# Performance work log

Measured on AMD Instinct MI355X. Metric: run time of the kernel, lower is better.

The kernel has to match this reference:

```python
import jax, jax.numpy as jnp
import numpy as np

B, C, H, W = 8, 512, 32, 32
N = H * W            # grid cells
G = 256              # num_groups
R = 9                # relations (self + 8 neighbors)
EPS = 1e-7           # module's self.eps
BN_EPS = 1e-5        # torch BatchNorm default eps


def setup_inputs() -> dict:
    key = jax.random.key(0)
    ks = jax.random.split(key, 10)
    inp = jax.random.normal(ks[0], (B, C, H, W), jnp.float32)
    group_label = jax.random.randint(ks[1], (B, N), 0, G)
    adj_mats = jax.random.uniform(ks[2], (R, N, N), jnp.float32)
    w1 = jax.random.normal(ks[3], (3, C, C), jnp.float32) * 0.02
    wg = jax.random.normal(ks[4], (3, R * C, R * C), jnp.float32) * 0.02
    w2 = jax.random.normal(ks[5], (3, C, C), jnp.float32) * 0.02
    bn_gamma = jnp.ones((3, 3, G), jnp.float32)
    bn_beta = jnp.zeros((3, 3, G), jnp.float32)
    conv_w = jax.random.normal(ks[6], (C, 2 * C), jnp.float32) * 0.02
    conv_b = jnp.zeros((C,), jnp.float32)
    return {"inp": inp, "group_label": group_label, "adj_mats": adj_mats,
            "w1": w1, "wg": wg, "w2": w2, "bn_gamma": bn_gamma,
            "bn_beta": bn_beta, "conv_w": conv_w, "conv_b": conv_b}


def _batchnorm(x, gamma, beta):
    # x: (B, G, C); BatchNorm1d(num_features=G): normalize over (B, C) per group
    mean = jnp.mean(x, axis=(0, 2), keepdims=True)
    var = jnp.var(x, axis=(0, 2), keepdims=True)
    return gamma[None, :, None] * (x - mean) * jax.lax.rsqrt(var + BN_EPS) + beta[None, :, None]


def _res_block(x, coef, w1, wg, w2, gam, bet):
    # x: (B, G, C); coef: (B, 9, G, G)
    h = x @ w1.T                                  # dense1 (no bias)
    h = jax.nn.relu(_batchnorm(h, gam[0], bet[0]))
    e = jnp.tile(h, (1, 1, R)) @ wg.T             # (B, G, 9C) graph_conv_1
    e = e.reshape(B, R, G, C)                     # same row-major reinterpret as torch
    h = jnp.einsum('brgh,brhc->bgc', coef, e)     # coef @ out, then sum over relations
    h = jax.nn.relu(_batchnorm(h, gam[1], bet[1]))
    h = h @ w2.T                                  # dense2 (no bias)
    h = _batchnorm(h, gam[2], bet[2]) + x
    return jax.nn.relu(h)


def reference(inp, group_label, adj_mats, w1, wg, w2, bn_gamma, bn_beta, conv_w, conv_b):
    gm = jax.nn.one_hot(group_label, G, dtype=inp.dtype)        # (B, N, G)
    # make_coef_matrix
    t = jnp.einsum('rnm,bmg->brng', adj_mats, gm)               # (B, 9, N, G)
    ga = jnp.einsum('brng,bnh->brgh', t, gm)                    # (B, 9, G, G)
    den = jax.nn.relu(ga - jnp.flip(ga, axis=0))                # flip over batch dim (as in source)
    den = den.at[:, 3].set(ga[:, 3])
    coef = den / (ga.sum(axis=3, keepdims=True) + 1.0)          # (B, 9, G, G)
    # pooling
    bar = gm / (gm.sum(axis=2, keepdims=True) + EPS)
    x = jnp.einsum('bcn,bng->bgc', inp.reshape(B, C, N), bar)   # (B, G, C)
    # three residual blocks
    for i in range(3):
        x = _res_block(x, coef, w1[i], wg[i], w2[i], bn_gamma[i], bn_beta[i])
    # unpooling
    tilde = gm / (gm.sum(axis=1, keepdims=True) + EPS)
    x = jnp.einsum('bng,bgc->bnc', tilde, x).reshape(B, C, H, W)  # raw reshape as in torch
    xcat = jnp.concatenate([x, inp], axis=1)                      # (B, 2C, H, W)
    out = jnp.einsum('bchw,oc->bohw', xcat, conv_w) + conv_b[None, :, None, None]
    return out
```

## Files before the change

### kernel.cpp

```cpp
#include <hip/hip_runtime.h>
#include <math.h>

using half8 = __attribute__((ext_vector_type(8))) _Float16;
using half4 = __attribute__((ext_vector_type(4))) _Float16;
using f32x4 = __attribute__((ext_vector_type(4))) float;

static constexpr size_t OFF_WGCH  = 0;
static constexpr size_t OFF_COEF  = 7077888;
static constexpr size_t OFF_COEFH = 11796480;
static constexpr size_t OFF_X     = 16515072;
static constexpr size_t OFF_CNTI  = 17565696;
static constexpr size_t OFF_LISTS = 17567744;
static constexpr size_t OFF_CSRO  = 17666048;
static constexpr size_t OFF_CSRV  = 17668352;
static constexpr size_t OFF_W1H   = 17672960;
static constexpr size_t OFF_W2H   = 18459392;
static constexpr size_t OFF_CWH   = 19245824;
static constexpr size_t OFF_XH    = 19770112;
static constexpr size_t OFF_HH    = 20818688;
static constexpr size_t OFF_BIG   = 21867264;
static constexpr size_t OFF_GA    = 40741632;
static constexpr size_t OFF_H1    = OFF_GA;
static constexpr size_t OFF_H2    = OFF_GA + 1048576;

__device__ inline void gll16(const void* g, void* l) {
  __builtin_amdgcn_global_load_lds(
      (__attribute__((address_space(1))) void*)(size_t)g,
      (__attribute__((address_space(3))) void*)(size_t)l, 16, 0, 0);
}

__global__ __launch_bounds__(256) void k_collapse_wg(const float* __restrict__ wg,
                                                     _Float16* __restrict__ whi) {
  size_t idx = (size_t)blockIdx.x * 256 + threadIdx.x;
  size_t i = idx / (4608u * 128u);
  size_t rem = idx % (4608u * 128u);
  size_t j = rem / 128u, c4 = rem % 128u;
  const float* p = wg + i * 21233664ull + j * 4608ull + c4 * 4;
  float4 s = {0.f, 0.f, 0.f, 0.f};
#pragma unroll
  for (int r = 0; r < 9; ++r) {
    float4 v = *(const float4*)(p + r * 512);
    s.x += v.x; s.y += v.y; s.z += v.z; s.w += v.w;
  }
  half4 hv;
  hv[0] = (_Float16)s.x; hv[1] = (_Float16)s.y;
  hv[2] = (_Float16)s.z; hv[3] = (_Float16)s.w;
  *(half4*)&whi[idx * 4] = hv;
}

__global__ __launch_bounds__(256) void k_split3(const float* __restrict__ w1,
                                                const float* __restrict__ w2,
                                                const float* __restrict__ cw,
                                                _Float16* __restrict__ w1h,
                                                _Float16* __restrict__ w2h,
                                                _Float16* __restrict__ cwh) {
  size_t idx = (size_t)blockIdx.x * 256 + threadIdx.x;
  if (idx < 786432) {
    w1h[idx] = (_Float16)w1[idx];
  } else if (idx < 1572864) {
    size_t o = idx - 786432;
    w2h[o] = (_Float16)w2[o];
  } else {
    size_t o = idx - 1572864;
    cwh[o] = (_Float16)cw[o];
  }
}

__global__ __launch_bounds__(256) void k_lists(const int* __restrict__ gl,
                                               int* __restrict__ cntI,
                                               int* __restrict__ lists) {
  int idx = blockIdx.x * 256 + threadIdx.x;
  int b = idx >> 10, n = idx & 1023;
  int h = gl[idx];
  int pos = atomicAdd(&cntI[b * 256 + h], 1);
  if (pos < 48) lists[(b * 256 + h) * 48 + pos] = n;
}

__global__ __launch_bounds__(256) void k_csr(const int* __restrict__ cntI,
                                             const int* __restrict__ lists,
                                             int* __restrict__ csr_off,
                                             unsigned short* __restrict__ csr_val) {
  __shared__ int wsum[256];
  __shared__ int tot[257];
  int t = threadIdx.x;
  int base = t * 8;
  int loc[8]; int s = 0;
#pragma unroll
  for (int i = 0; i < 8; ++i) {
    int c = cntI[base + i]; if (c > 48) c = 48;
    loc[i] = s; s += c;
  }
  wsum[t] = s;
  __syncthreads();
  if (t == 0) {
    int a = 0;
    for (int i = 0; i < 256; ++i) { tot[i] = a; a += wsum[i]; }
    tot[256] = a;
  }
  __syncthreads();
  int off0 = tot[t];
#pragma unroll
  for (int i = 0; i < 8; ++i) {
    int bg = base + i;
    int o = off0 + loc[i];
    csr_off[bg] = o;
    int c = cntI[bg]; if (c > 48) c = 48;
    for (int j = 0; j < c; ++j)
      csr_val[o + j] = (unsigned short)(lists[bg * 48 + j] & 1023);
  }
  if (t == 0) csr_off[2048] = tot[256];
}

__global__ __launch_bounds__(256) void k_t2ga(const float* __restrict__ adj,
                                              const int* __restrict__ cntI,
                                              const int* __restrict__ lists,
                                              float* __restrict__ gaT) {
  __shared__ float ul[9][1024];
  __shared__ int lsh[48];
  int t = threadIdx.x;
  int b = blockIdx.x >> 8, h = blockIdx.x & 255;
  int cnt = cntI[b * 256 + h]; if (cnt > 48) cnt = 48;
  if (t < cnt) lsh[t] = lists[(b * 256 + h) * 48 + t];
  __syncthreads();
  float u[9][4];
#pragma unroll
  for (int r = 0; r < 9; ++r)
#pragma unroll
    for (int j = 0; j < 4; ++j) u[r][j] = 0.f;
  for (int i = 0; i < cnt; ++i) {
    const float* base = adj + ((size_t)lsh[i] << 10) + t;
#pragma unroll
    for (int r = 0; r < 9; ++r) {
      const float* p = base + (size_t)r * 1048576;
      u[r][0] += p[0];
      u[r][1] += p[256];
      u[r][2] += p[512];
      u[r][3] += p[768];
    }
  }
#pragma unroll
  for (int r = 0; r < 9; ++r)
#pragma unroll
    for (int j = 0; j < 4; ++j) ul[r][j * 256 + t] = u[r][j];
  __syncthreads();
  int g = t;
  int cg = cntI[b * 256 + g]; if (cg > 48) cg = 48;
  const int* lg = lists + (b * 256 + g) * 48;
  float s[9];
#pragma unroll
  for (int r = 0; r < 9; ++r) s[r] = 0.f;
  for (int i = 0; i < cg; ++i) {
    int m = lg[i];
#pragma unroll
    for (int r = 0; r < 9; ++r) s[r] += ul[r][m];
  }
#pragma unroll
  for (int r = 0; r < 9; ++r)
    gaT[(((size_t)(b * 9 + r)) * 256 + h) * 256 + g] = s[r];
}

__global__ __launch_bounds__(256) void k_gasum(const float* __restrict__ gaT,
                                               float* __restrict__ rowsum) {
  int z = blockIdx.x;
  int t = threadIdx.x;
  const float* p = gaT + ((size_t)z * 256) * 256 + t;
  float s = 0.f;
  for (int h = 0; h < 256; ++h) s += p[(size_t)h * 256];
  rowsum[z * 256 + t] = s;
}

__global__ __launch_bounds__(256) void k_coef_t(const float* __restrict__ gaT,
                                                const float* __restrict__ rowsum,
                                                _Float16* __restrict__ chi) {
  __shared__ float tl[64][65];
  __shared__ float tlf[64][65];
  __shared__ float rs[64];
  int t = threadIdx.x;
  int z = blockIdx.y;
  int b = z / 9, r = z % 9;
  int tile = blockIdx.x;
  int h0 = (tile & 3) * 64, g0 = (tile >> 2) * 64;
  size_t base  = ((size_t)z * 256 + h0) * 256 + g0;
  size_t baseF = ((size_t)((7 - b) * 9 + r) * 256 + h0) * 256 + g0;
  for (int k = t; k < 4096; k += 256) {
    int i = k >> 6, j = k & 63;
    tl[i][j]  = gaT[base  + (size_t)i * 256 + j];
    tlf[i][j] = gaT[baseF + (size_t)i * 256 + j];
  }
  if (t < 64) rs[t] = rowsum[z * 256 + g0 + t] + 1.0f;
  __syncthreads();
  for (int k = t; k < 4096; k += 256) {
    int i2 = k >> 6, j2 = k & 63;
    float v = tl[j2][i2], vf = tlf[j2][i2];
    float num = (r == 3) ? v : fmaxf(v - vf, 0.f);
    float c = num / rs[i2];
    size_t o = ((size_t)z * 256 + g0 + i2) * 256 + h0 + j2;
    chi[o] = (_Float16)c;
  }
}

__global__ __launch_bounds__(256) void k_pool_csr(const float* __restrict__ inp,
                                                  const int* __restrict__ csr_off,
                                                  const unsigned short* __restrict__ csr_val,
                                                  float* __restrict__ x,
                                                  _Float16* __restrict__ xh) {
  __shared__ float rows[8][1032];
  __shared__ int offs[257];
  __shared__ unsigned short vals[1024];
  int t = threadIdx.x;
  int b = blockIdx.x >> 6, cch = blockIdx.x & 63;
  const float4* src = (const float4*)(inp + (size_t)b * 524288 + (size_t)cch * 8 * 1024);
  for (int k = t; k < 2048; k += 256) {
    float4 v = src[k];
    int c = k >> 8;
    int m = (k & 255) << 2;
    *(float4*)&rows[c][m] = v;
  }
  for (int k = t; k < 257; k += 256) offs[k] = csr_off[b * 256 + k];
  __syncthreads();
  int vbase = offs[0];
  int nv = offs[256] - vbase;
  for (int k = t; k < nv; k += 256) vals[k] = csr_val[vbase + k];
  __syncthreads();
  int g = t;
  int o0 = offs[g] - vbase, o1 = offs[g + 1] - vbase;
  float s[8] = {0.f, 0.f, 0.f, 0.f, 0.f, 0.f, 0.f, 0.f};
  for (int i = o0; i < o1; ++i) {
    int n = vals[i];
#pragma unroll
    for (int c = 0; c < 8; ++c) s[c] += rows[c][n];
  }
  const float sc = 1.0f / (1.0f + 1e-7f);
  size_t xbase = ((size_t)b * 256 + g) * 512 + cch * 8;
#pragma unroll
  for (int c = 0; c < 8; ++c) {
    float v = s[c] * sc;
    x[xbase + c] = v;
    xh[xbase + c] = (_Float16)v;
  }
}

__global__ __launch_bounds__(256) void k_mfma_nt1f(const _Float16* __restrict__ Ahi,
                                                   const _Float16* __restrict__ Bhi,
                                                   float* __restrict__ C,
                                                   const float* __restrict__ bias,
                                                   int M, int N, int K,
                                                   size_t Bbs, size_t Cbs) {
  __shared__ __align__(16) _Float16 Ash[2][128][32];
  __shared__ __align__(16) _Float16 Bsh[2][64][32];
  int tid = threadIdx.x;
  int z = blockIdx.z;
  const _Float16* Bh = Bhi + (size_t)z * Bbs;
  float* Cz = C + (size_t)z * Cbs;
  int bm = blockIdx.y * 128, bn = blockIdx.x * 64;
  int w = tid >> 6, lane = tid & 63;
  int wr = w >> 1, wc = w & 1;
  int l15 = lane & 15, l4 = lane >> 4;
  int rsub = lane >> 2;
  int qk = (lane & 3) * 8;
  int ar = w * 16 + rsub;
  int ar2 = ar + 64;
  f32x4 acc[4][2];
#pragma unroll
  for (int m = 0; m < 4; ++m)
#pragma unroll
    for (int n = 0; n < 2; ++n) acc[m][n] = (f32x4){0.f, 0.f, 0.f, 0.f};
  auto STG = [&](int bi, int k0) {
    gll16(Ahi + (size_t)(bm + ar) * K + k0 + qk,  &Ash[bi][w * 16][0]);
    gll16(Ahi + (size_t)(bm + ar2) * K + k0 + qk, &Ash[bi][w * 16 + 64][0]);
    gll16(Bh + (size_t)(bn + ar) * K + k0 + qk,   &Bsh[bi][w * 16][0]);
  };
  int nt = K >> 5;
  STG(0, 0);
  int cur = 0;
  for (int t = 0; t < nt; ++t, cur ^= 1) {
    __syncthreads();
    if (t + 1 < nt) STG(cur ^ 1, (t + 1) << 5);
    half8 afh[4], bfh[2];
#pragma unroll
    for (int m = 0; m < 4; ++m)
      afh[m] = *(const half8*)&Ash[cur][wr * 64 + m * 16 + l15][l4 * 8];
#pragma unroll
    for (int n = 0; n < 2; ++n)
      bfh[n] = *(const half8*)&Bsh[cur][wc * 32 + n * 16 + l15][l4 * 8];
#pragma unroll
    for (int m = 0; m < 4; ++m)
#pragma unroll
      for (int n = 0; n < 2; ++n)
        acc[m][n] = __builtin_amdgcn_mfma_f32_16x16x32_f16(afh[m], bfh[n], acc[m][n], 0, 0, 0);
  }
#pragma unroll
  for (int m = 0; m < 4; ++m)
#pragma unroll
    for (int n = 0; n < 2; ++n)
#pragma unroll
      for (int rr = 0; rr < 4; ++rr) {
        int row = bm + wr * 64 + m * 16 + l4 * 4 + rr;
        int col = bn + wc * 32 + n * 16 + l15;
        float v = acc[m][n][rr];
        if (bias) v += bias[row];
        Cz[(size_t)row * N + col] = v;
      }
}

__global__ __launch_bounds__(256) void k_mfma_nt1f_64(const _Float16* __restrict__ Ahi,
                                                      const _Float16* __restrict__ Bhi,
                                                      _Float16* __restrict__ C,
                                                      int M, int N, int K) {
  __shared__ __align__(16) _Float16 Ash[2][64][32];
  __shared__ __align__(16) _Float16 Bsh[2][64][32];
  int tid = threadIdx.x;
  int bm = blockIdx.y * 64, bn = blockIdx.x * 64;
  int w = tid >> 6, lane = tid & 63;
  int wr = w >> 1, wc = w & 1;
  int l15 = lane & 15, l4 = lane >> 4;
  int rsub = lane >> 2;
  int qk = (lane & 3) * 8;
  int ar = w * 16 + rsub;
  f32x4 acc[2][2];
#pragma unroll
  for (int m = 0; m < 2; ++m)
#pragma unroll
    for (int n = 0; n < 2; ++n) acc[m][n] = (f32x4){0.f, 0.f, 0.f, 0.f};
  auto STG = [&](int bi, int k0) {
    gll16(Ahi + (size_t)(bm + ar) * K + k0 + qk, &Ash[bi][w * 16][0]);
    gll16(Bhi + (size_t)(bn + ar) * K + k0 + qk, &Bsh[bi][w * 16][0]);
  };
  int nt = K >> 5;
  STG(0, 0);
  int cur = 0;
  for (int t = 0; t < nt; ++t, cur ^= 1) {
    __syncthreads();
    if (t + 1 < nt) STG(cur ^ 1, (t + 1) << 5);
    half8 afh[2], bfh[2];
#pragma unroll
    for (int m = 0; m < 2; ++m)
      afh[m] = *(const half8*)&Ash[cur][wr * 32 + m * 16 + l15][l4 * 8];
#pragma unroll
    for (int n = 0; n < 2; ++n)
      bfh[n] = *(const half8*)&Bsh[cur][wc * 32 + n * 16 + l15][l4 * 8];
#pragma unroll
    for (int m = 0; m < 2; ++m)
#pragma unroll
      for (int n = 0; n < 2; ++n)
        acc[m][n] = __builtin_amdgcn_mfma_f32_16x16x32_f16(afh[m], bfh[n], acc[m][n], 0, 0, 0);
  }
#pragma unroll
  for (int m = 0; m < 2; ++m)
#pragma unroll
    for (int n = 0; n < 2; ++n)
#pragma unroll
      for (int rr = 0; rr < 4; ++rr) {
        int row = bm + wr * 32 + m * 16 + l4 * 4 + rr;
        int col = bn + wc * 32 + n * 16 + l15;
        C[(size_t)row * N + col] = (_Float16)acc[m][n][rr];
      }
}

__global__ __launch_bounds__(256) void k_mfma_nt1f_128(const _Float16* __restrict__ Ahi,
                                                       const _Float16* __restrict__ Bhi,
                                                       _Float16* __restrict__ C,
                                                       int M, int N, int K) {
  __shared__ __align__(16) _Float16 Ash[2][128][32];
  __shared__ __align__(16) _Float16 Bsh[2][128][32];
  int tid = threadIdx.x;
  int bm = blockIdx.y * 128, bn = blockIdx.x * 128;
  int w = tid >> 6, lane = tid & 63;
  int wr = w >> 1, wc = w & 1;
  int l15 = lane & 15, l4 = lane >> 4;
  int rsub = lane >> 2;
  int qk = (lane & 3) * 8;
  int ar = w * 16 + rsub;
  int ar2 = ar + 64;
  f32x4 acc[4][4];
#pragma unroll
  for (int m = 0; m < 4; ++m)
#pragma unroll
    for (int n = 0; n < 4; ++n) acc[m][n] = (f32x4){0.f, 0.f, 0.f, 0.f};
  auto STG = [&](int bi, int k0) {
    gll16(Ahi + (size_t)(bm + ar) * K + k0 + qk,  &Ash[bi][w * 16][0]);
    gll16(Ahi + (size_t)(bm + ar2) * K + k0 + qk, &Ash[bi][w * 16 + 64][0]);
    gll16(Bhi + (size_t)(bn + ar) * K + k0 + qk,  &Bsh[bi][w * 16][0]);
    gll16(Bhi + (size_t)(bn + ar2) * K + k0 + qk, &Bsh[bi][w * 16 + 64][0]);
  };
  int nt = K >> 5;
  STG(0, 0);
  int cur = 0;
  for (int t = 0; t < nt; ++t, cur ^= 1) {
    __syncthreads();
    if (t + 1 < nt) STG(cur ^ 1, (t + 1) << 5);
    half8 afh[4], bfh[4];
#pragma unroll
    for (int m = 0; m < 4; ++m)
      afh[m] = *(const half8*)&Ash[cur][wr * 64 + m * 16 + l15][l4 * 8];
#pragma unroll
    for (int n = 0; n < 4; ++n)
      bfh[n] = *(const half8*)&Bsh[cur][wc * 64 + n * 16 + l15][l4 * 8];
#pragma unroll
    for (int m = 0; m < 4; ++m)
#pragma unroll
      for (int n = 0; n < 4; ++n)
        acc[m][n] = __builtin_amdgcn_mfma_f32_16x16x32_f16(afh[m], bfh[n], acc[m][n], 0, 0, 0);
  }
#pragma unroll
  for (int m = 0; m < 4; ++m)
#pragma unroll
    for (int n = 0; n < 4; ++n)
#pragma unroll
      for (int rr = 0; rr < 4; ++rr) {
        int row = bm + wr * 64 + m * 16 + l4 * 4 + rr;
        int col = bn + wc * 64 + n * 16 + l15;
        C[(size_t)row * N + col] = (_Float16)acc[m][n][rr];
      }
}

__global__ __launch_bounds__(256) void k_eT_split(const _Float16* __restrict__ e,
                                                  _Float16* __restrict__ eth) {
  __shared__ _Float16 tl[64][72];
  int t = threadIdx.x;
  int z = blockIdx.z;
  int b = z / 9, r = z % 9;
  int h0 = blockIdx.y * 64, c0 = blockIdx.x * 64;
  const _Float16* ez = e + (size_t)b * 1179648 + (size_t)r * 131072;
  for (int k = t; k < 4096; k += 256) {
    int i = k >> 6, j = k & 63;
    tl[i][j] = ez[(size_t)(h0 + i) * 512 + c0 + j];
  }
  __syncthreads();
  for (int k = t; k < 4096; k += 256) {
    int i = k >> 6, j = k & 63;
    size_t o = ((size_t)z * 512 + c0 + i) * 256 + h0 + j;
    eth[o] = tl[j][i];
  }
}

__global__ __launch_bounds__(256) void k_einsum_mfma(const _Float16* __restrict__ Ahi,
                                                     const _Float16* __restrict__ Bhi,
                                                     _Float16* __restrict__ h2) {
  __shared__ __align__(16) _Float16 Ash[2][64][32];
  __shared__ __align__(16) _Float16 Bsh[2][64][32];
  int tid = threadIdx.x;
  int b = blockIdx.z;
  int bm = blockIdx.y * 64, bn = blockIdx.x * 64;
  int w = tid >> 6, lane = tid & 63;
  int wr = w >> 1, wc = w & 1;
  int l15 = lane & 15, l4 = lane >> 4;
  int rsub = lane >> 2;
  int qk = (lane & 3) * 8;
  int ar = w * 16 + rsub;
  f32x4 acc[2][2];
#pragma unroll
  for (int m = 0; m < 2; ++m)
#pragma unroll
    for (int n = 0; n < 2; ++n) acc[m][n] = (f32x4){0.f, 0.f, 0.f, 0.f};
  auto STG = [&](int bi, int kk) {
    int r = kk >> 3, k0 = (kk & 7) << 5;
    const _Float16* Ah = Ahi + ((size_t)b * 9 + r) * 65536 + (size_t)(bm + ar) * 256 + k0 + qk;
    const _Float16* Bh = Bhi + ((size_t)b * 9 + r) * 131072 + (size_t)(bn + ar) * 256 + k0 + qk;
    gll16(Ah, &Ash[bi][w * 16][0]);
    gll16(Bh, &Bsh[bi][w * 16][0]);
  };
  STG(0, 0);
  int cur = 0;
  for (int kk = 0; kk < 72; ++kk, cur ^= 1) {
    __syncthreads();
    if (kk + 1 < 72) STG(cur ^ 1, kk + 1);
    half8 afh[2], bfh[2];
#pragma unroll
    for (int m = 0; m < 2; ++m)
      afh[m] = *(const half8*)&Ash[cur][wr * 32 + m * 16 + l15][l4 * 8];
#pragma unroll
    for (int n = 0; n < 2; ++n)
      bfh[n] = *(const half8*)&Bsh[cur][wc * 32 + n * 16 + l15][l4 * 8];
#pragma unroll
    for (int m = 0; m < 2; ++m)
#pragma unroll
      for (int n = 0; n < 2; ++n)
        acc[m][n] = __builtin_amdgcn_mfma_f32_16x16x32_f16(afh[m], bfh[n], acc[m][n], 0, 0, 0);
  }
#pragma unroll
  for (int m = 0; m < 2; ++m)
#pragma unroll
    for (int n = 0; n < 2; ++n)
#pragma unroll
      for (int rr = 0; rr < 4; ++rr) {
        int row = bm + wr * 32 + m * 16 + l4 * 4 + rr;
        int col = bn + wc * 32 + n * 16 + l15;
        h2[(size_t)b * 131072 + (size_t)row * 512 + col] = (_Float16)acc[m][n][rr];
      }
}

__global__ __launch_bounds__(256) void k_bn_fused(const _Float16* __restrict__ h,
                                                  const float* __restrict__ gamma,
                                                  const float* __restrict__ beta,
                                                  float* __restrict__ x,
                                                  _Float16* __restrict__ ohi,
                                                  int res) {
  __shared__ double ls[256], lq[256];
  __shared__ float bc[2];
  int g = blockIdx.x;
  int tid = threadIdx.x;
  float v[16];
  double s = 0.0, q = 0.0;
#pragma unroll
  for (int i = 0; i < 16; ++i) {
    int idx = i * 256 + tid;
    int bb = idx >> 9, c = idx & 511;
    float f = (float)h[((size_t)(bb * 256 + g) << 9) + c];
    v[i] = f;
    double d = (double)f;
    s += d; q += d * d;
  }
  ls[tid] = s; lq[tid] = q;
  __syncthreads();
  for (int off = 128; off; off >>= 1) {
    if (tid < off) { ls[tid] += ls[tid + off]; lq[tid] += lq[tid + off]; }
    __syncthreads();
  }
  if (tid == 0) {
    double mean = ls[0] * (1.0 / 4096.0);
    double var = lq[0] * (1.0 / 4096.0) - mean * mean;
    if (var < 0.0) var = 0.0;
    float rstd = (float)rsqrt(var + 1e-5);
    float a = gamma[g] * rstd;
    bc[0] = a;
    bc[1] = beta[g] - (float)mean * a;
  }
  __syncthreads();
  float a = bc[0], b2 = bc[1];
#pragma unroll
  for (int i = 0; i < 16; ++i) {
    int idx = i * 256 + tid;
    int bb = idx >> 9, c = idx & 511;
    size_t o = ((size_t)(bb * 256 + g) << 9) + c;
    float y = fmaf(v[i], a, b2);
    if (res) y += x[o];
    y = fmaxf(y, 0.f);
    if (res) x[o] = y;
    ohi[o] = (_Float16)y;
  }
}

__global__ __launch_bounds__(256) void k_xcatT(const float* __restrict__ x,
                                               const int* __restrict__ cntI,
                                               const int* __restrict__ gl,
                                               const float* __restrict__ inp,
                                               _Float16* __restrict__ xch) {
  __shared__ float tl[64][65];
  __shared__ int lab[1024];
  __shared__ float ic[256];
  int t = threadIdx.x;
  int b = blockIdx.y, p0 = blockIdx.x * 64;
  if (blockIdx.z == 0) {
    for (int k = t; k < 1024; k += 256) lab[k] = gl[b * 1024 + k];
    if (t < 256) ic[t] = 1.0f / ((float)cntI[b * 256 + t] + 1e-7f);
    __syncthreads();
    for (int pp = 0; pp < 64; ++pp) {
      int p = p0 + pp;
      int p9 = p >> 9, c2 = p & 511;
      const float* xb = x + (size_t)b * 131072 + c2;
      size_t obase = ((size_t)b * 1024 + p) * 1024;
#pragma unroll
      for (int ch = 0; ch < 512; ch += 256) {
        int c = ch + t;
        int g = lab[2 * c + p9];
        xch[obase + c] = (_Float16)(xb[(size_t)g * 512] * ic[g]);
      }
    }
  } else {
    for (int ct = 0; ct < 512; ct += 64) {
      __syncthreads();
      for (int k = t; k < 4096; k += 256) {
        int i = k >> 6, j = k & 63;
        tl[i][j] = inp[(size_t)b * 524288 + (size_t)(ct + i) * 1024 + p0 + j];
      }
      __syncthreads();
      for (int k = t; k < 4096; k += 256) {
        int i = k >> 6, j = k & 63;
        size_t o = ((size_t)b * 1024 + p0 + i) * 1024 + 512 + ct + j;
        xch[o] = (_Float16)tl[j][i];
      }
    }
  }
}

extern "C" void kernel_launch(void* const* d_in, const int* in_sizes, int n_in,
                              void* d_out, int out_size, void* d_ws, size_t ws_size,
                              hipStream_t stream) {
  const float* inp   = (const float*)d_in[0];
  const int*   gl    = (const int*)d_in[1];
  const float* adj   = (const float*)d_in[2];
  const float* w1    = (const float*)d_in[3];
  const float* wg    = (const float*)d_in[4];
  const float* w2    = (const float*)d_in[5];
  const float* bng   = (const float*)d_in[6];
  const float* bnb   = (const float*)d_in[7];
  const float* convw = (const float*)d_in[8];
  const float* convb = (const float*)d_in[9];
  float* out = (float*)d_out;
  float* ws = (float*)d_ws;

  _Float16* wgchi = (_Float16*)(ws + OFF_WGCH);
  _Float16* coefhi = (_Float16*)(ws + OFF_COEFH);
  float* rowsum = ws + OFF_COEF;
  float* x     = ws + OFF_X;
  int*   cntI  = (int*)(ws + OFF_CNTI);
  int*   lists = (int*)(ws + OFF_LISTS);
  int*   csrO  = (int*)(ws + OFF_CSRO);
  unsigned short* csrV = (unsigned short*)(ws + OFF_CSRV);
  _Float16* w1hi = (_Float16*)(ws + OFF_W1H);
  _Float16* w2hi = (_Float16*)(ws + OFF_W2H);
  _Float16* cwhi = (_Float16*)(ws + OFF_CWH);
  _Float16* xhi  = (_Float16*)(ws + OFF_XH);
  _Float16* hhi  = (_Float16*)(ws + OFF_HH);
  _Float16* e_h  = (_Float16*)(ws + OFF_BIG);
  _Float16* eth  = (_Float16*)(ws + OFF_BIG + 4718592);
  _Float16* xch  = (_Float16*)(ws + OFF_BIG);
  float* gaT = ws + OFF_GA;
  _Float16* h1h = (_Float16*)(ws + OFF_H1);
  _Float16* h2h = (_Float16*)(ws + OFF_H2);

  hipMemsetAsync(cntI, 0, 2048 * 4, stream);

  k_collapse_wg<<<6912, 256, 0, stream>>>(wg, wgchi);
  k_split3<<<8192, 256, 0, stream>>>(w1, w2, convw, w1hi, w2hi, cwhi);
  k_lists<<<32, 256, 0, stream>>>(gl, cntI, lists);
  k_csr<<<1, 256, 0, stream>>>(cntI, lists, csrO, csrV);
  k_t2ga<<<2048, 256, 0, stream>>>(adj, cntI, lists, gaT);
  k_gasum<<<72, 256, 0, stream>>>(gaT, rowsum);
  k_coef_t<<<dim3(16, 72), 256, 0, stream>>>(gaT, rowsum, coefhi);
  k_pool_csr<<<512, 256, 0, stream>>>(inp, csrO, csrV, x, xhi);

  for (int i = 0; i < 3; ++i) {
    k_mfma_nt1f_64<<<dim3(8, 32), 256, 0, stream>>>(xhi, w1hi + (size_t)i * 262144,
        h1h, 2048, 512, 512);
    k_bn_fused<<<256, 256, 0, stream>>>(h1h, bng + (i * 3 + 0) * 256, bnb + (i * 3 + 0) * 256,
        nullptr, hhi, 0);
    k_mfma_nt1f_128<<<dim3(36, 16), 256, 0, stream>>>(hhi, wgchi + (size_t)i * 2359296,
        e_h, 2048, 4608, 512);
    k_eT_split<<<dim3(8, 4, 72), 256, 0, stream>>>(e_h, eth);
    k_einsum_mfma<<<dim3(8, 4, 8), 256, 0, stream>>>(coefhi, eth, h2h);
    k_bn_fused<<<256, 256, 0, stream>>>(h2h, bng + (i * 3 + 1) * 256, bnb + (i * 3 + 1) * 256,
        nullptr, hhi, 0);
    k_mfma_nt1f_64<<<dim3(8, 32), 256, 0, stream>>>(hhi, w2hi + (size_t)i * 262144,
        h1h, 2048, 512, 512);
    k_bn_fused<<<256, 256, 0, stream>>>(h1h, bng + (i * 3 + 2) * 256, bnb + (i * 3 + 2) * 256,
        x, xhi, 1);
  }

  k_xcatT<<<dim3(16, 8, 2), 256, 0, stream>>>(x, cntI, gl, inp, xch);
  k_mfma_nt1f<<<dim3(16, 4, 8), 256, 0, stream>>>(cwhi, xch, out, convb,
      512, 1024, 1024, 1048576, 524288);
}
```

Before: 478.8 us.

## Double K-step per stage in MFMA GEMMs and merge weight prep kernels

All four MFMA GEMM kernels now stage 64 K-elements per pipeline step, as two 32-wide sub-tiles, instead of 32. This halves the number of __syncthreads barriers and loop iterations and gives each wave more MFMA work per barrier. The cost is double the LDS footprint, which can lower occupancy. Separately, the wg-collapse and weight-cast kernels are merged into one launch to save a kernel launch.

```diff
diff --git a/kernel.cpp b/kernel.cpp
--- a/kernel.cpp
+++ b/kernel.cpp
@@ -29,40 +29,42 @@
       (__attribute__((address_space(3))) void*)(size_t)l, 16, 0, 0);
 }
 
-__global__ __launch_bounds__(256) void k_collapse_wg(const float* __restrict__ wg,
-                                                     _Float16* __restrict__ whi) {
-  size_t idx = (size_t)blockIdx.x * 256 + threadIdx.x;
-  size_t i = idx / (4608u * 128u);
-  size_t rem = idx % (4608u * 128u);
-  size_t j = rem / 128u, c4 = rem % 128u;
-  const float* p = wg + i * 21233664ull + j * 4608ull + c4 * 4;
-  float4 s = {0.f, 0.f, 0.f, 0.f};
-#pragma unroll
-  for (int r = 0; r < 9; ++r) {
-    float4 v = *(const float4*)(p + r * 512);
-    s.x += v.x; s.y += v.y; s.z += v.z; s.w += v.w;
-  }
-  half4 hv;
-  hv[0] = (_Float16)s.x; hv[1] = (_Float16)s.y;
-  hv[2] = (_Float16)s.z; hv[3] = (_Float16)s.w;
-  *(half4*)&whi[idx * 4] = hv;
-}
-
-__global__ __launch_bounds__(256) void k_split3(const float* __restrict__ w1,
+__global__ __launch_bounds__(256) void k_prep_w(const float* __restrict__ wg,
+                                                const float* __restrict__ w1,
                                                 const float* __restrict__ w2,
                                                 const float* __restrict__ cw,
+                                                _Float16* __restrict__ wgh,
                                                 _Float16* __restrict__ w1h,
                                                 _Float16* __restrict__ w2h,
                                                 _Float16* __restrict__ cwh) {
-  size_t idx = (size_t)blockIdx.x * 256 + threadIdx.x;
-  if (idx < 786432) {
-    w1h[idx] = (_Float16)w1[idx];
-  } else if (idx < 1572864) {
-    size_t o = idx - 786432;
-    w2h[o] = (_Float16)w2[o];
+  int bid = blockIdx.x;
+  if (bid < 6912) {
+    size_t idx = (size_t)bid * 256 + threadIdx.x;
+    size_t i = idx / (4608u * 128u);
+    size_t rem = idx % (4608u * 128u);
+    size_t j = rem / 128u, c4 = rem % 128u;
+    const float* p = wg + i * 21233664ull + j * 4608ull + c4 * 4;
+    float4 s = {0.f, 0.f, 0.f, 0.f};
+#pragma unroll
+    for (int r = 0; r < 9; ++r) {
+      float4 v = *(const float4*)(p + r * 512);
+      s.x += v.x; s.y += v.y; s.z += v.z; s.w += v.w;
+    }
+    half4 hv;
+    hv[0] = (_Float16)s.x; hv[1] = (_Float16)s.y;
+    hv[2] = (_Float16)s.z; hv[3] = (_Float16)s.w;
+    *(half4*)&wgh[idx * 4] = hv;
   } else {
-    size_t o = idx - 1572864;
-    cwh[o] = (_Float16)cw[o];
+    size_t idx = (size_t)(bid - 6912) * 256 + threadIdx.x;
+    if (idx < 786432) {
+      w1h[idx] = (_Float16)w1[idx];
+    } else if (idx < 1572864) {
+      size_t o = idx - 786432;
+      w2h[o] = (_Float16)w2[o];
+    } else {
+      size_t o = idx - 1572864;
+      cwh[o] = (_Float16)cw[o];
+    }
   }
 }
 
@@ -246,8 +248,8 @@
                                                    const float* __restrict__ bias,
                                                    int M, int N, int K,
                                                    size_t Bbs, size_t Cbs) {
-  __shared__ __align__(16) _Float16 Ash[2][128][32];
-  __shared__ __align__(16) _Float16 Bsh[2][64][32];
+  __shared__ __align__(16) _Float16 Ash[2][2][128][32];
+  __shared__ __align__(16) _Float16 Bsh[2][2][64][32];
   int tid = threadIdx.x;
   int z = blockIdx.z;
   const _Float16* Bh = Bhi + (size_t)z * Bbs;
@@ -266,28 +268,35 @@
 #pragma unroll
     for (int n = 0; n < 2; ++n) acc[m][n] = (f32x4){0.f, 0.f, 0.f, 0.f};
   auto STG = [&](int bi, int k0) {
-    gll16(Ahi + (size_t)(bm + ar) * K + k0 + qk,  &Ash[bi][w * 16][0]);
-    gll16(Ahi + (size_t)(bm + ar2) * K + k0 + qk, &Ash[bi][w * 16 + 64][0]);
-    gll16(Bh + (size_t)(bn + ar) * K + k0 + qk,   &Bsh[bi][w * 16][0]);
+#pragma unroll
+    for (int ks = 0; ks < 2; ++ks) {
+      int kk = k0 + ks * 32;
+      gll16(Ahi + (size_t)(bm + ar) * K + kk + qk,  &Ash[bi][ks][w * 16][0]);
+      gll16(Ahi + (size_t)(bm + ar2) * K + kk + qk, &Ash[bi][ks][w * 16 + 64][0]);
+      gll16(Bh + (size_t)(bn + ar) * K + kk + qk,   &Bsh[bi][ks][w * 16][0]);
+    }
   };
-  int nt = K >> 5;
+  int nt = K >> 6;
   STG(0, 0);
   int cur = 0;
   for (int t = 0; t < nt; ++t, cur ^= 1) {
     __syncthreads();
-    if (t + 1 < nt) STG(cur ^ 1, (t + 1) << 5);
-    half8 afh[4], bfh[2];
-#pragma unroll
-    for (int m = 0; m < 4; ++m)
-      afh[m] = *(const half8*)&Ash[cur][wr * 64 + m * 16 + l15][l4 * 8];
-#pragma unroll
-    for (int n = 0; n < 2; ++n)
-      bfh[n] = *(const half8*)&Bsh[cur][wc * 32 + n * 16 + l15][l4 * 8];
-#pragma unroll
-    for (int m = 0; m < 4; ++m)
+    if (t + 1 < nt) STG(cur ^ 1, (t + 1) << 6);
+#pragma unroll
+    for (int ks = 0; ks < 2; ++ks) {
+      half8 afh[4], bfh[2];
+#pragma unroll
+      for (int m = 0; m < 4; ++m)
+        afh[m] = *(const half8*)&Ash[cur][ks][wr * 64 + m * 16 + l15][l4 * 8];
 #pragma unroll
       for (int n = 0; n < 2; ++n)
-        acc[m][n] = __builtin_amdgcn_mfma_f32_16x16x32_f16(afh[m], bfh[n], acc[m][n], 0, 0, 0);
+        bfh[n] = *(const half8*)&Bsh[cur][ks][wc * 32 + n * 16 + l15][l4 * 8];
+#pragma unroll
+      for (int m = 0; m < 4; ++m)
+#pragma unroll
+        for (int n = 0; n < 2; ++n)
+          acc[m][n] = __builtin_amdgcn_mfma_f32_16x16x32_f16(afh[m], bfh[n], acc[m][n], 0, 0, 0);
+    }
   }
 #pragma unroll
   for (int m = 0; m < 4; ++m)
@@ -307,8 +316,8 @@
                                                       const _Float16* __restrict__ Bhi,
                                                       _Float16* __restrict__ C,
                                                       int M, int N, int K) {
-  __shared__ __align__(16) _Float16 Ash[2][64][32];
-  __shared__ __align__(16) _Float16 Bsh[2][64][32];
+  __shared__ __align__(16) _Float16 Ash[2][2][64][32];
+  __shared__ __align__(16) _Float16 Bsh[2][2][64][32];
   int tid = threadIdx.x;
   int bm = blockIdx.y * 64, bn = blockIdx.x * 64;
   int w = tid >> 6, lane = tid & 63;
@@ -323,27 +332,34 @@
 #pragma unroll
     for (int n = 0; n < 2; ++n) acc[m][n] = (f32x4){0.f, 0.f, 0.f, 0.f};
   auto STG = [&](int bi, int k0) {
-    gll16(Ahi + (size_t)(bm + ar) * K + k0 + qk, &Ash[bi][w * 16][0]);
-    gll16(Bhi + (size_t)(bn + ar) * K + k0 + qk, &Bsh[bi][w * 16][0]);
+#pragma unroll
+    for (int ks = 0; ks < 2; ++ks) {
+      int kk = k0 + ks * 32;
+      gll16(Ahi + (size_t)(bm + ar) * K + kk + qk, &Ash[bi][ks][w * 16][0]);
+      gll16(Bhi + (size_t)(bn + ar) * K + kk + qk, &Bsh[bi][ks][w * 16][0]);
+    }
   };
-  int nt = K >> 5;
+  int nt = K >> 6;
   STG(0, 0);
   int cur = 0;
   for (int t = 0; t < nt; ++t, cur ^= 1) {
     __syncthreads();
-    if (t + 1 < nt) STG(cur ^ 1, (t + 1) << 5);
-    half8 afh[2], bfh[2];
-#pragma unroll
-    for (int m = 0; m < 2; ++m)
-      afh[m] = *(const half8*)&Ash[cur][wr * 32 + m * 16 + l15][l4 * 8];
-#pragma unroll
-    for (int n = 0; n < 2; ++n)
-      bfh[n] = *(const half8*)&Bsh[cur][wc * 32 + n * 16 + l15][l4 * 8];
-#pragma unroll
-    for (int m = 0; m < 2; ++m)
+    if (t + 1 < nt) STG(cur ^ 1, (t + 1) << 6);
+#pragma unroll
+    for (int ks = 0; ks < 2; ++ks) {
+      half8 afh[2], bfh[2];
+#pragma unroll
+      for (int m = 0; m < 2; ++m)
+        afh[m] = *(const half8*)&Ash[cur][ks][wr * 32 + m * 16 + l15][l4 * 8];
 #pragma unroll
       for (int n = 0; n < 2; ++n)
-        acc[m][n] = __builtin_amdgcn_mfma_f32_16x16x32_f16(afh[m], bfh[n], acc[m][n], 0, 0, 0);
+        bfh[n] = *(const half8*)&Bsh[cur][ks][wc * 32 + n * 16 + l15][l4 * 8];
+#pragma unroll
+      for (int m = 0; m < 2; ++m)
+#pragma unroll
+        for (int n = 0; n < 2; ++n)
+          acc[m][n] = __builtin_amdgcn_mfma_f32_16x16x32_f16(afh[m], bfh[n], acc[m][n], 0, 0, 0);
+    }
   }
 #pragma unroll
   for (int m = 0; m < 2; ++m)
@@ -361,8 +377,8 @@
                                                        const _Float16* __restrict__ Bhi,
                                                        _Float16* __restrict__ C,
                                                        int M, int N, int K) {
-  __shared__ __align__(16) _Float16 Ash[2][128][32];
-  __shared__ __align__(16) _Float16 Bsh[2][128][32];
+  __shared__ __align__(16) _Float16 Ash[2][2][128][32];
+  __shared__ __align__(16) _Float16 Bsh[2][2][128][32];
   int tid = threadIdx.x;
   int bm = blockIdx.y * 128, bn = blockIdx.x * 128;
   int w = tid >> 6, lane = tid & 63;
@@ -378,29 +394,36 @@
 #pragma unroll
     for (int n = 0; n < 4; ++n) acc[m][n] = (f32x4){0.f, 0.f, 0.f, 0.f};
   auto STG = [&](int bi, int k0) {
-    gll16(Ahi + (size_t)(bm + ar) * K + k0 + qk,  &Ash[bi][w * 16][0]);
-    gll16(Ahi + (size_t)(bm + ar2) * K + k0 + qk, &Ash[bi][w * 16 + 64][0]);
-    gll16(Bhi + (size_t)(bn + ar) * K + k0 + qk,  &Bsh[bi][w * 16][0]);
-    gll16(Bhi + (size_t)(bn + ar2) * K + k0 + qk, &Bsh[bi][w * 16 + 64][0]);
+#pragma unroll
+    for (int ks = 0; ks < 2; ++ks) {
+      int kk = k0 + ks * 32;
+      gll16(Ahi + (size_t)(bm + ar) * K + kk + qk,  &Ash[bi][ks][w * 16][0]);
+      gll16(Ahi + (size_t)(bm + ar2) * K + kk + qk, &Ash[bi][ks][w * 16 + 64][0]);
+      gll16(Bhi + (size_t)(bn + ar) * K + kk + qk,  &Bsh[bi][ks][w * 16][0]);
+      gll16(Bhi + (size_t)(bn + ar2) * K + kk + qk, &Bsh[bi][ks][w * 16 + 64][0]);
+    }
   };
-  int nt = K >> 5;
+  int nt = K >> 6;
   STG(0, 0);
   int cur = 0;
   for (int t = 0; t < nt; ++t, cur ^= 1) {
     __syncthreads();
-    if (t + 1 < nt) STG(cur ^ 1, (t + 1) << 5);
-    half8 afh[4], bfh[4];
-#pragma unroll
-    for (int m = 0; m < 4; ++m)
-      afh[m] = *(const half8*)&Ash[cur][wr * 64 + m * 16 + l15][l4 * 8];
-#pragma unroll
-    for (int n = 0; n < 4; ++n)
-      bfh[n] = *(const half8*)&Bsh[cur][wc * 64 + n * 16 + l15][l4 * 8];
-#pragma unroll
-    for (int m = 0; m < 4; ++m)
+    if (t + 1 < nt) STG(cur ^ 1, (t + 1) << 6);
+#pragma unroll
+    for (int ks = 0; ks < 2; ++ks) {
+      half8 afh[4], bfh[4];
+#pragma unroll
+      for (int m = 0; m < 4; ++m)
+        afh[m] = *(const half8*)&Ash[cur][ks][wr * 64 + m * 16 + l15][l4 * 8];
 #pragma unroll
       for (int n = 0; n < 4; ++n)
-        acc[m][n] = __builtin_amdgcn_mfma_f32_16x16x32_f16(afh[m], bfh[n], acc[m][n], 0, 0, 0);
+        bfh[n] = *(const half8*)&Bsh[cur][ks][wc * 64 + n * 16 + l15][l4 * 8];
+#pragma unroll
+      for (int m = 0; m < 4; ++m)
+#pragma unroll
+        for (int n = 0; n < 4; ++n)
+          acc[m][n] = __builtin_amdgcn_mfma_f32_16x16x32_f16(afh[m], bfh[n], acc[m][n], 0, 0, 0);
+    }
   }
 #pragma unroll
   for (int m = 0; m < 4; ++m)
@@ -437,8 +460,8 @@
 __global__ __launch_bounds__(256) void k_einsum_mfma(const _Float16* __restrict__ Ahi,
                                                      const _Float16* __restrict__ Bhi,
                                                      _Float16* __restrict__ h2) {
-  __shared__ __align__(16) _Float16 Ash[2][64][32];
-  __shared__ __align__(16) _Float16 Bsh[2][64][32];
+  __shared__ __align__(16) _Float16 Ash[2][2][64][32];
+  __shared__ __align__(16) _Float16 Bsh[2][2][64][32];
   int tid = threadIdx.x;
   int b = blockIdx.z;
   int bm = blockIdx.y * 64, bn = blockIdx.x * 64;
@@ -454,29 +477,35 @@
 #pragma unroll
     for (int n = 0; n < 2; ++n) acc[m][n] = (f32x4){0.f, 0.f, 0.f, 0.f};
   auto STG = [&](int bi, int kk) {
-    int r = kk >> 3, k0 = (kk & 7) << 5;
+    int r = kk >> 2, k0 = (kk & 3) << 6;
     const _Float16* Ah = Ahi + ((size_t)b * 9 + r) * 65536 + (size_t)(bm + ar) * 256 + k0 + qk;
     const _Float16* Bh = Bhi + ((size_t)b * 9 + r) * 131072 + (size_t)(bn + ar) * 256 + k0 + qk;
-    gll16(Ah, &Ash[bi][w * 16][0]);
-    gll16(Bh, &Bsh[bi][w * 16][0]);
+#pragma unroll
+    for (int ks = 0; ks < 2; ++ks) {
+      gll16(Ah + ks * 32, &Ash[bi][ks][w * 16][0]);
+      gll16(Bh + ks * 32, &Bsh[bi][ks][w * 16][0]);
+    }
   };
   STG(0, 0);
   int cur = 0;
-  for (int kk = 0; kk < 72; ++kk, cur ^= 1) {
+  for (int kk = 0; kk < 36; ++kk, cur ^= 1) {
     __syncthreads();
-    if (kk + 1 < 72) STG(cur ^ 1, kk + 1);
-    half8 afh[2], bfh[2];
-#pragma unroll
-    for (int m = 0; m < 2; ++m)
-      afh[m] = *(const half8*)&Ash[cur][wr * 32 + m * 16 + l15][l4 * 8];
-#pragma unroll
-    for (int n = 0; n < 2; ++n)
-      bfh[n] = *(const half8*)&Bsh[cur][wc * 32 + n * 16 + l15][l4 * 8];
-#pragma unroll
-    for (int m = 0; m < 2; ++m)
+    if (kk + 1 < 36) STG(cur ^ 1, kk + 1);
+#pragma unroll
+    for (int ks = 0; ks < 2; ++ks) {
+      half8 afh[2], bfh[2];
+#pragma unroll
+      for (int m = 0; m < 2; ++m)
+        afh[m] = *(const half8*)&Ash[cur][ks][wr * 32 + m * 16 + l15][l4 * 8];
 #pragma unroll
       for (int n = 0; n < 2; ++n)
-        acc[m][n] = __builtin_amdgcn_mfma_f32_16x16x32_f16(afh[m], bfh[n], acc[m][n], 0, 0, 0);
+        bfh[n] = *(const half8*)&Bsh[cur][ks][wc * 32 + n * 16 + l15][l4 * 8];
+#pragma unroll
+      for (int m = 0; m < 2; ++m)
+#pragma unroll
+        for (int n = 0; n < 2; ++n)
+          acc[m][n] = __builtin_amdgcn_mfma_f32_16x16x32_f16(afh[m], bfh[n], acc[m][n], 0, 0, 0);
+    }
   }
 #pragma unroll
   for (int m = 0; m < 2; ++m)
@@ -622,8 +651,7 @@
 
   hipMemsetAsync(cntI, 0, 2048 * 4, stream);
 
-  k_collapse_wg<<<6912, 256, 0, stream>>>(wg, wgchi);
-  k_split3<<<8192, 256, 0, stream>>>(w1, w2, convw, w1hi, w2hi, cwhi);
+  k_prep_w<<<15104, 256, 0, stream>>>(wg, w1, w2, convw, wgchi, w1hi, w2hi, cwhi);
   k_lists<<<32, 256, 0, stream>>>(gl, cntI, lists);
   k_csr<<<1, 256, 0, stream>>>(cntI, lists, csrO, csrV);
   k_t2ga<<<2048, 256, 0, stream>>>(adj, cntI, lists, gaT);
```

Result: faster. 463.6 us (-3.2%).
